# Kernel optimization log

Measured on AMD Instinct MI355X. Metric: run time of the kernel, lower is better.

Reference implementation:

```python
import jax, jax.numpy as jnp
import numpy as np

B, CIN, COUT, KH, KW = 8, 64, 128, 3, 3
H = W = 64
STRIDE, PAD = 1, 1
G = 1  # deformable groups


def setup_inputs() -> dict:
    key = jax.random.key(0)
    k1, k2, k3 = jax.random.split(key, 3)
    rgb = jax.random.normal(k1, (B, CIN, H, W), dtype=jnp.float32)
    # torchvision layout: [B, 2*G*KH*KW, Ho, Wo], (dy, dx) pairs per kernel tap
    offsets = jax.random.normal(k2, (B, 2 * G * KH * KW, H, W), dtype=jnp.float32)
    # xavier_uniform for weight [COUT, CIN, KH, KW]
    fan_in, fan_out = CIN * KH * KW, COUT * KH * KW
    a = float(np.sqrt(6.0 / (fan_in + fan_out)))
    weight = jax.random.uniform(k3, (COUT, CIN, KH, KW), dtype=jnp.float32, minval=-a, maxval=a)
    bias = jnp.zeros((COUT,), dtype=jnp.float32)
    return {"rgb": rgb, "offsets": offsets, "weight": weight, "bias": bias}


def _deform_conv2d(rgb, offsets, weight, bias):
    b, cin, h, w = rgb.shape
    cout, _, kh, kw = weight.shape
    K = kh * kw
    ho = (h + 2 * PAD - kh) // STRIDE + 1
    wo = (w + 2 * PAD - kw) // STRIDE + 1
    cg = cin // G  # channels per deformable group

    off = offsets.reshape(b, G, K, 2, ho, wo)
    dy, dx = off[:, :, :, 0], off[:, :, :, 1]  # [b, G, K, ho, wo]

    ky, kx = jnp.meshgrid(jnp.arange(kh), jnp.arange(kw), indexing="ij")
    ky = ky.reshape(K).astype(jnp.float32)
    kx = kx.reshape(K).astype(jnp.float32)
    base_y = (jnp.arange(ho) * STRIDE - PAD).astype(jnp.float32)
    base_x = (jnp.arange(wo) * STRIDE - PAD).astype(jnp.float32)

    # sampling coordinates: p0 + kernel tap + learned offset -> [b, G, K, ho, wo]
    y = base_y[None, None, None, :, None] + ky[None, None, :, None, None] + dy
    x = base_x[None, None, None, None, :] + kx[None, None, :, None, None] + dx

    y0 = jnp.floor(y)
    x0 = jnp.floor(x)
    fy = y - y0
    fx = x - x0
    y0i = y0.astype(jnp.int32)
    x0i = x0.astype(jnp.int32)

    x_flat = rgb.reshape(b, G, cg, h * w)
    P = K * ho * wo

    def gather_corner(yc, xc, wgt):
        valid = (yc >= 0) & (yc < h) & (xc >= 0) & (xc < w)
        idx = jnp.clip(yc, 0, h - 1) * w + jnp.clip(xc, 0, w - 1)
        wgt = jnp.where(valid, wgt, 0.0).reshape(b, G, 1, P)
        vals = jnp.take_along_axis(x_flat, idx.reshape(b, G, 1, P), axis=3)
        return vals * wgt

    col = (
        gather_corner(y0i, x0i, (1 - fy) * (1 - fx))
        + gather_corner(y0i, x0i + 1, (1 - fy) * fx)
        + gather_corner(y0i + 1, x0i, fy * (1 - fx))
        + gather_corner(y0i + 1, x0i + 1, fy * fx)
    )  # [b, G, cg, K*ho*wo]

    col = col.reshape(b, cin * K, ho * wo)
    out = jnp.einsum("ok,bkp->bop", weight.reshape(cout, cin * K), col)
    return out.reshape(b, cout, ho, wo) + bias[None, :, None, None]


def reference(rgb, offsets, weight, bias):
    return _deform_conv2d(rgb, offsets, weight, bias)
```

## Files before the change

### kernel.cpp

```cpp
#include <hip/hip_runtime.h>

#define COUT_  128
#define KP     1024
#define CAPR   20
#define IMGC   (21 * 64)
#define IMGBUF (4 * IMGC)
#define COLU   36
#define COLBUF (64 * COLU)

#if __has_builtin(__builtin_amdgcn_fdot2_f32_bf16)
#define HAS_DOT2 1
#else
#define HAS_DOT2 0
#endif

typedef __attribute__((ext_vector_type(8))) __bf16 bf16x8;
typedef __attribute__((ext_vector_type(2))) __bf16 bf16x2;
typedef unsigned short u16x8 __attribute__((ext_vector_type(8)));
typedef __attribute__((ext_vector_type(4))) float f32x4;

__device__ __forceinline__ unsigned int f2bf(float f) {
    union { float f; unsigned int u; } c; c.f = f;
    unsigned int u = c.u;
    u += 0x7fffu + ((u >> 16) & 1u);
    return u >> 16;
}
__device__ __forceinline__ float bitsf(unsigned int u) {
    union { unsigned int u; float f; } c; c.u = u; return c.f;
}
__device__ __forceinline__ unsigned int pk2bf(float lo, float hi) {
    bf16x2 v;
    v[0] = (__bf16)lo;
    v[1] = (__bf16)hi;
    return __builtin_bit_cast(unsigned int, v);
}
__device__ __forceinline__ bf16x2 mk_bf2(float lo, float hi) {
    bf16x2 v;
    v[0] = (__bf16)lo;
    v[1] = (__bf16)hi;
    return v;
}

__global__ void prep_w(const float* __restrict__ w, unsigned short* __restrict__ wbf) {
    const int base = (blockIdx.x * 256 + threadIdx.x) * 4;
    const int cout = base >> 10, r = base & 1023;
    const int quad = r >> 6, j2 = r & 63;
    const int k = j2 >> 2;
    ushort4 v = make_ushort4(0, 0, 0, 0);
    if (k < 9) {
        const float* wp = w + (cout * 64 + quad * 4) * 9 + k;
        v.x = (unsigned short)f2bf(wp[0]);
        v.y = (unsigned short)f2bf(wp[9]);
        v.z = (unsigned short)f2bf(wp[18]);
        v.w = (unsigned short)f2bf(wp[27]);
    }
    *(ushort4*)(wbf + base) = v;
}

__launch_bounds__(256, 2)
__global__ void deform_mfma6(const float* __restrict__ rgb,
                             const float* __restrict__ off,
                             const unsigned short* __restrict__ wbf,
                             const float* __restrict__ bias,
                             float* __restrict__ out) {
    __shared__ unsigned int S[2 * COLBUF + 2 * IMGBUF];
    __shared__ int sW[8];
    unsigned int* imgU = S + 2 * COLBUF;

    const int t    = threadIdx.x;
    const int bid  = blockIdx.x;
    const int b    = bid & 7;
    const int ho   = bid >> 3;
    const int lane = t & 63;
    const int wv   = t >> 6;
    const int px   = lane;
    const int ln15 = lane & 15;
    const int q    = lane >> 4;

    const float* offb = off + b * (2 * 9 * 4096);

    float m_fy[3], m_fx[3]; int m_y0[3], m_x0[3];
    int lmin = 64, lmax = -1;
#pragma unroll
    for (int ti = 0; ti < 3; ti++) {
        const int kt = (ti < 2) ? (wv + ti * 4) : 8;
        const float dy = offb[((2 * kt)     * 64 + ho) * 64 + px];
        const float dx = offb[((2 * kt + 1) * 64 + ho) * 64 + px];
        const float y = (float)(ho - 1 + kt / 3) + dy;
        const float x = (float)(px - 1 + kt % 3) + dx;
        const float y0f = floorf(y), x0f = floorf(x);
        m_fy[ti] = y - y0f; m_fx[ti] = x - x0f;
        m_y0[ti] = (int)y0f; m_x0[ti] = (int)x0f;
        const int r0 = min(max(m_y0[ti], 0), 63), r1 = min(max(m_y0[ti] + 1, 0), 63);
        lmin = min(lmin, r0); lmax = max(lmax, r1);
    }
#pragma unroll
    for (int d = 1; d < 64; d <<= 1) {
        lmin = min(lmin, __shfl_xor(lmin, d));
        lmax = max(lmax, __shfl_xor(lmax, d));
    }
    if (lane == 0) { sW[wv] = lmin; sW[4 + wv] = lmax; }
    __syncthreads();
    const int ymin  = min(min(sW[0], sW[1]), min(sW[2], sW[3]));
    const int ymax  = max(max(sW[4], sW[5]), max(sW[6], sW[7]));
    const int nrows = ymax - ymin + 1;
    const int nr4   = min((nrows + 3) & ~3, CAPR);
    const int ymin2 = max(0, min(ymin, 64 - nr4));

    {
        const uint4 z4 = make_uint4(0, 0, 0, 0);
        for (int i = t; i < 512; i += 256) {
            const int buf = i >> 8, j = i & 255, p_ = j >> 2, r = j & 3;
            *(uint4*)&S[buf * COLBUF + p_ * COLU + 16 + r * 4] = z4;
        }
        if (t < 128) {
            const int buf = t >> 6, pl = (t >> 4) & 3, c4 = t & 15;
            *(uint4*)&imgU[buf * IMGBUF + pl * IMGC + nr4 * 64 + c4 * 4] = z4;
        }
    }

    float4 sv[5];
    auto stage_load = [&](int gg) {
        const float* gp = rgb + ((unsigned)(b * 64 + gg * 4 + wv) * 64 + ymin2 + (lane >> 4)) * 64 + (lane & 15) * 4;
#pragma unroll
        for (int n = 0; n < 5; n++)
            if (n * 4 < nr4) sv[n] = *(const float4*)(gp + n * 4 * 64);
    };
    auto stage_write = [&](int gg) {
        unsigned int* lp = imgU + (gg & 1) * IMGBUF + wv * IMGC + (lane >> 4) * 64 + (lane & 15) * 4;
#pragma unroll
        for (int n = 0; n < 5; n++) {
            if (n * 4 < nr4) {
                const float4 v = sv[n];
                float nf = __shfl(v.x, lane + 1);
                if ((lane & 15) == 15) nf = 0.f;
                uint4 pk;
                pk.x = pk2bf(v.x, v.y); pk.y = pk2bf(v.y, v.z);
                pk.z = pk2bf(v.z, v.w); pk.w = pk2bf(v.w, nf);
                *(uint4*)(lp + n * 4 * 64) = pk;
            }
        }
    };

    int ma[3];
#if HAS_DOT2
    bf16x2 wtp[3], wbp[3];
#else
    float mw[3][4];
#endif
#pragma unroll
    for (int ti = 0; ti < 3; ti++) {
        const int y0 = m_y0[ti], x0 = m_x0[ti];
        const float fy = m_fy[ti], fx = m_fx[ti];
        const int r0 = y0 - ymin2;
        const float wy0 = (y0 >= 0  && y0 < 64) ? (1.f - fy) : 0.f;
        const float wy1 = (y0 >= -1 && y0 < 63) ? fy         : 0.f;
        const bool ylo = (r0 < 0);
        const float wtop = ylo ? wy1 : wy0;
        const float wbot = ylo ? 0.f : wy1;
        const int r0c = ylo ? 0 : min(r0, nr4 - 1);
        const float wx0 = (x0 >= 0  && x0 < 64) ? (1.f - fx) : 0.f;
        const float wx1 = (x0 >= -1 && x0 < 63) ? fx         : 0.f;
        const bool xlo = (x0 < 0);
        const float wA = xlo ? wx1 : wx0;
        const float wB = xlo ? 0.f : wx1;
        const int xc = min(max(x0, 0), 63);
        ma[ti] = r0c * 64 + xc;
#if HAS_DOT2
        wtp[ti] = mk_bf2(wtop * wA, wtop * wB);
        wbp[ti] = mk_bf2(wbot * wA, wbot * wB);
#else
        mw[ti][0] = wtop * wA; mw[ti][1] = wtop * wB;
        mw[ti][2] = wbot * wA; mw[ti][3] = wbot * wB;
#endif
    }

    f32x4 acc[2][4] = {};
    const unsigned short* wrow0 = wbf + (wv * 32 + ln15) * KP;
    const unsigned short* wrow1 = wrow0 + 16 * KP;
    const unsigned short* col16 = (const unsigned short*)S;

    auto interp1 = [&](const unsigned int* pl, int ti) -> float {
        const unsigned int* p = pl + ma[ti];
        const unsigned int tp = p[0];
        const unsigned int bp = p[64];
#if HAS_DOT2
        float r = __builtin_amdgcn_fdot2_f32_bf16(__builtin_bit_cast(bf16x2, tp), wtp[ti], 0.f, false);
        return  __builtin_amdgcn_fdot2_f32_bf16(__builtin_bit_cast(bf16x2, bp), wbp[ti], r, false);
#else
        return mw[ti][0] * bitsf(tp << 16) + mw[ti][1] * bitsf(tp & 0xffff0000u)
             + mw[ti][2] * bitsf(bp << 16) + mw[ti][3] * bitsf(bp & 0xffff0000u);
#endif
    };
    auto gather = [&](int g) {
        const unsigned int* ib = imgU + (g & 1) * IMGBUF;
        unsigned int* cb = S + (g & 1) * COLBUF + px * COLU;
#pragma unroll
        for (int ti = 0; ti < 2; ti++) {
            const int kt = wv + ti * 4;
            uint2 w2;
            w2.x = pk2bf(interp1(ib, ti),            interp1(ib + IMGC, ti));
            w2.y = pk2bf(interp1(ib + 2 * IMGC, ti), interp1(ib + 3 * IMGC, ti));
            *(uint2*)&cb[kt * 2] = w2;
        }
        if (wv == (g & 3))
            cb[16] = pk2bf(interp1(ib, 2),            interp1(ib + IMGC, 2));
        if (wv == ((g + 2) & 3))
            cb[17] = pk2bf(interp1(ib + 2 * IMGC, 2), interp1(ib + 3 * IMGC, 2));
    };
    auto mfma_steps = [&](int gg) {
#pragma unroll
        for (int sg = 0; sg < 2; sg++) {
            const int s = 2 * gg + sg;
            const u16x8 a0u = *(const u16x8*)(wrow0 + s * 32 + q * 8);
            const u16x8 a1u = *(const u16x8*)(wrow1 + s * 32 + q * 8);
            const bf16x8 a0 = __builtin_bit_cast(bf16x8, a0u);
            const bf16x8 a1 = __builtin_bit_cast(bf16x8, a1u);
#pragma unroll
            for (int nj = 0; nj < 4; nj++) {
                const u16x8 bu = *(const u16x8*)(col16 + (gg & 1) * (COLBUF * 2)
                                                 + (nj * 16 + ln15) * (COLU * 2) + sg * 32 + q * 8);
                const bf16x8 bv = __builtin_bit_cast(bf16x8, bu);
                acc[0][nj] = __builtin_amdgcn_mfma_f32_16x16x32_bf16(a0, bv, acc[0][nj], 0, 0, 0);
                acc[1][nj] = __builtin_amdgcn_mfma_f32_16x16x32_bf16(a1, bv, acc[1][nj], 0, 0, 0);
            }
        }
    };

    stage_load(0); stage_write(0);
    __syncthreads();

    for (int g = 0; g < 16; g++) {
        if (g + 1 < 16) stage_load(g + 1);
        gather(g);
        if (g > 0) mfma_steps(g - 1);
        if (g + 1 < 16) stage_write(g + 1);
        __syncthreads();
    }
    mfma_steps(15);

#pragma unroll
    for (int mi = 0; mi < 2; mi++) {
#pragma unroll
        for (int r = 0; r < 4; r++) {
            const int cout = wv * 32 + mi * 16 + q * 4 + r;
            const float bv = bias[cout];
            float* orow = out + ((b * COUT_ + cout) * 64 + ho) * 64;
#pragma unroll
            for (int nj = 0; nj < 4; nj++)
                orow[nj * 16 + ln15] = acc[mi][nj][r] + bv;
        }
    }
}

extern "C" void kernel_launch(void* const* d_in, const int* in_sizes, int n_in,
                              void* d_out, int out_size, void* d_ws, size_t ws_size,
                              hipStream_t stream) {
    const float* rgb  = (const float*)d_in[0];
    const float* off  = (const float*)d_in[1];
    const float* w    = (const float*)d_in[2];
    const float* bias = (const float*)d_in[3];
    float* out = (float*)d_out;
    unsigned short* wbf = (unsigned short*)d_ws;

    prep_w<<<COUT_ * KP / 1024, 256, 0, stream>>>(w, wbf);
    deform_mfma6<<<512, 256, 0, stream>>>(rgb, off, wbf, bias, out);
}
```

Baseline: 97.36 us.

## Double-buffer global image loads in registers and use lightweight LDS barrier

The main loop is unrolled by two so each global load of an input channel group is issued two iterations ahead into alternating register sets (svA/svB), giving loads more time in flight. The first two loads are hoisted ahead of the LDS zero-initialisation and bilinear-weight setup. __syncthreads is replaced by a custom barrier that waits only on LDS counters (lgkmcnt) with sched_barrier fences, so pending global loads need not drain at each barrier. This costs extra registers and could lower occupancy.

```diff
diff --git a/kernel.cpp b/kernel.cpp
--- a/kernel.cpp
+++ b/kernel.cpp
@@ -39,6 +39,13 @@
     v[0] = (__bf16)lo;
     v[1] = (__bf16)hi;
     return v;
+}
+
+__device__ __forceinline__ void barx() {
+    __builtin_amdgcn_sched_barrier(0);
+    asm volatile("s_waitcnt lgkmcnt(0)" ::: "memory");
+    __builtin_amdgcn_s_barrier();
+    __builtin_amdgcn_sched_barrier(0);
 }
 
 __global__ void prep_w(const float* __restrict__ w, unsigned short* __restrict__ wbf) {
@@ -107,26 +114,14 @@
     const int nr4   = min((nrows + 3) & ~3, CAPR);
     const int ymin2 = max(0, min(ymin, 64 - nr4));
 
-    {
-        const uint4 z4 = make_uint4(0, 0, 0, 0);
-        for (int i = t; i < 512; i += 256) {
-            const int buf = i >> 8, j = i & 255, p_ = j >> 2, r = j & 3;
-            *(uint4*)&S[buf * COLBUF + p_ * COLU + 16 + r * 4] = z4;
-        }
-        if (t < 128) {
-            const int buf = t >> 6, pl = (t >> 4) & 3, c4 = t & 15;
-            *(uint4*)&imgU[buf * IMGBUF + pl * IMGC + nr4 * 64 + c4 * 4] = z4;
-        }
-    }
-
-    float4 sv[5];
-    auto stage_load = [&](int gg) {
+    float4 svA[5], svB[5];
+    auto stage_load = [&](int gg, float4 (&sv)[5]) {
         const float* gp = rgb + ((unsigned)(b * 64 + gg * 4 + wv) * 64 + ymin2 + (lane >> 4)) * 64 + (lane & 15) * 4;
 #pragma unroll
         for (int n = 0; n < 5; n++)
             if (n * 4 < nr4) sv[n] = *(const float4*)(gp + n * 4 * 64);
     };
-    auto stage_write = [&](int gg) {
+    auto stage_write = [&](int gg, float4 (&sv)[5]) {
         unsigned int* lp = imgU + (gg & 1) * IMGBUF + wv * IMGC + (lane >> 4) * 64 + (lane & 15) * 4;
 #pragma unroll
         for (int n = 0; n < 5; n++) {
@@ -141,6 +136,21 @@
             }
         }
     };
+
+    stage_load(0, svA);
+    stage_load(1, svB);
+
+    {
+        const uint4 z4 = make_uint4(0, 0, 0, 0);
+        for (int i = t; i < 512; i += 256) {
+            const int buf = i >> 8, j = i & 255, p_ = j >> 2, r = j & 3;
+            *(uint4*)&S[buf * COLBUF + p_ * COLU + 16 + r * 4] = z4;
+        }
+        if (t < 128) {
+            const int buf = t >> 6, pl = (t >> 4) & 3, c4 = t & 15;
+            *(uint4*)&imgU[buf * IMGBUF + pl * IMGC + nr4 * 64 + c4 * 4] = z4;
+        }
+    }
 
     int ma[3];
 #if HAS_DOT2
@@ -227,15 +237,20 @@
         }
     };
 
-    stage_load(0); stage_write(0);
-    __syncthreads();
-
-    for (int g = 0; g < 16; g++) {
-        if (g + 1 < 16) stage_load(g + 1);
+    stage_write(0, svA);
+    barx();
+
+    for (int g = 0; g < 16; g += 2) {
+        if (g + 2 < 16) stage_load(g + 2, svA);
         gather(g);
         if (g > 0) mfma_steps(g - 1);
-        if (g + 1 < 16) stage_write(g + 1);
-        __syncthreads();
+        stage_write(g + 1, svB);
+        barx();
+        if (g + 3 < 16) stage_load(g + 3, svB);
+        gather(g + 1);
+        mfma_steps(g);
+        if (g + 2 < 16) stage_write(g + 2, svA);
+        barx();
     }
     mfma_steps(15);
 
```

After: 95.48 us. No clear change (-1.9%).
